# Kernel optimization log

Measured on AMD Instinct MI355X. Metric: run time of the kernel, lower is better.

Reference implementation:

```python
import jax, jax.numpy as jnp
import numpy as np

# dims: B graphs of n nodes each (equal-size batch, matching ptr)
B, NPG, DIN, DEMB, EPN = 16, 2048, 128, 64, 16
N = B * NPG
E = N * EPN
GAMMA = 5.0   # DGM ln gamma (temperature on normalized affinities)
STD = 0.01    # noise std


def _entmax15_core(z):
    # exact 1.5-entmax along last axis (Peters & Martins), sort-based threshold
    z = 0.5 * z
    z = z - jnp.max(z, axis=-1, keepdims=True)
    zs = jnp.sort(z, axis=-1)[..., ::-1]                  # descending
    k = z.shape[-1]
    rho = jnp.arange(1, k + 1, dtype=z.dtype)
    mean = jnp.cumsum(zs, axis=-1) / rho
    meansq = jnp.cumsum(zs * zs, axis=-1) / rho
    ss = rho * (meansq - jnp.square(mean))
    delta = (1.0 - ss) / rho
    tau = mean - jnp.sqrt(jnp.clip(delta, 0.0))
    support = jnp.sum((tau <= zs).astype(jnp.int32), axis=-1, keepdims=True)
    tau_star = jnp.take_along_axis(tau, support - 1, axis=-1)
    return jnp.square(jnp.clip(z - tau_star, 0.0))


@jax.custom_vjp
def entmax15(z):
    return _entmax15_core(z)

def _e_fwd(z):
    y = _entmax15_core(z)
    return y, y

def _e_bwd(y, dy):
    g = jnp.sqrt(y)
    dz = dy * g
    q = jnp.sum(dz, axis=-1, keepdims=True) / jnp.sum(g, axis=-1, keepdims=True)
    return (dz - q * g,)

entmax15.defvjp(_e_fwd, _e_bwd)


def setup_inputs() -> dict:
    key = jax.random.key(0)
    ks = jax.random.split(key, 6)
    x = jax.random.normal(ks[0], (N, DIN), dtype=jnp.float32)
    # intra-graph random edges: local ids + per-graph offset
    g = jax.random.randint(ks[1], (2, E), 0, NPG)
    off = jnp.repeat(jnp.arange(B, dtype=jnp.int64) * NPG, E // B)
    edge_index = (g.astype(jnp.int64) + off[None, :])
    batch = jnp.repeat(jnp.arange(B, dtype=jnp.int64), NPG)
    ptr = jnp.arange(B + 1, dtype=jnp.int64) * NPG
    W_self = jax.random.normal(ks[2], (DIN, DEMB), dtype=jnp.float32) / np.sqrt(DIN).astype(np.float32)
    W_nei = jax.random.normal(ks[3], (DIN, DEMB), dtype=jnp.float32) / np.sqrt(DIN).astype(np.float32)
    b = jnp.zeros((DEMB,), dtype=jnp.float32)
    noise = jax.random.normal(ks[4], (B, NPG, NPG), dtype=jnp.float32) * STD
    return {"x": x, "edge_index": edge_index, "batch": batch, "ptr": ptr,
            "W_self": W_self, "W_nei": W_nei, "b": b, "noise": noise}


def reference(x, edge_index, batch, ptr, W_self, W_nei, b, noise):
    Ntot = x.shape[0]
    Bn = ptr.shape[0] - 1
    n = Ntot // Bn
    src, dst = edge_index[0], edge_index[1]
    # embed_f: one mean-aggregation GCN layer
    h = x @ W_self
    msg = (x @ W_nei)[src]
    agg = jax.ops.segment_sum(msg, dst, num_segments=Ntot)
    deg = jax.ops.segment_sum(jnp.ones((src.shape[0],), x.dtype), dst, num_segments=Ntot)
    x_aux = jax.nn.relu(h + agg / jnp.clip(deg, 1.0)[:, None] + b)
    # per-graph pairwise euclidean distance (equal-size graphs -> [B,n,d])
    xb = x_aux.reshape(Bn, n, -1)
    sq = jnp.sum(xb * xb, axis=-1)
    d2 = sq[:, :, None] + sq[:, None, :] - 2.0 * jnp.einsum('bnd,bmd->bnm', xb, xb)
    D = jnp.sqrt(jnp.clip(d2, 0.0) + 1e-12)
    logits = -D + noise                              # noisy negative distances
    mu = jnp.mean(logits, axis=-1, keepdims=True)    # ln = LayerNorm(gamma)
    sd = jnp.std(logits, axis=-1, keepdims=True)
    A = entmax15(GAMMA * (logits - mu) / (sd + 1e-5))  # sparse edge probs [B,n,n]
    logprobs = jnp.log(A + 1e-6)
    return x_aux, A, logprobs
```

## Files before the change

### kernel.cpp

```cpp
#include <hip/hip_runtime.h>

#define NGRAPH 16
#define NPG    2048
#define NNODE  (NGRAPH*NPG)
#define DIN    128
#define DEMB   64
#define NEDGE  (NNODE*16)
#define QCAP   4096

__device__ __forceinline__ float wsum(float v) {
    #pragma unroll
    for (int m = 1; m < 64; m <<= 1) v += __shfl_xor(v, m, 64);
    return v;
}
__device__ __forceinline__ float wmax(float v) {
    #pragma unroll
    for (int m = 1; m < 64; m <<= 1) v = fmaxf(v, __shfl_xor(v, m, 64));
    return v;
}

__global__ __launch_bounds__(256) void k_inproj(
    const float* __restrict__ x, const float* __restrict__ Wself,
    const float* __restrict__ Wnei, float* __restrict__ h, float* __restrict__ xn)
{
    __shared__ float ws[DIN*DEMB];
    __shared__ float wn[DIN*DEMB];
    int tid = threadIdx.x;
    int n0 = blockIdx.x * 32;
    #pragma unroll
    for (int k = 0; k < 8; ++k) {
        ((float4*)ws)[tid + k*256] = ((const float4*)Wself)[tid + k*256];
        ((float4*)wn)[tid + k*256] = ((const float4*)Wnei)[tid + k*256];
    }
    __syncthreads();
    int nl = tid >> 3, og = (tid & 7) * 8;
    const float* xr = x + (size_t)(n0 + nl) * DIN;
    float ah[8] = {0,0,0,0,0,0,0,0};
    float an[8] = {0,0,0,0,0,0,0,0};
    for (int d4 = 0; d4 < DIN/4; ++d4) {
        float4 xv = *(const float4*)(xr + d4*4);
        #pragma unroll
        for (int dd = 0; dd < 4; ++dd) {
            float xs = (dd==0)?xv.x:(dd==1)?xv.y:(dd==2)?xv.z:xv.w;
            int d = d4*4 + dd;
            float4 a = *(const float4*)&ws[d*DEMB + og];
            float4 b = *(const float4*)&ws[d*DEMB + og + 4];
            ah[0] += xs*a.x; ah[1] += xs*a.y; ah[2] += xs*a.z; ah[3] += xs*a.w;
            ah[4] += xs*b.x; ah[5] += xs*b.y; ah[6] += xs*b.z; ah[7] += xs*b.w;
            float4 c = *(const float4*)&wn[d*DEMB + og];
            float4 e = *(const float4*)&wn[d*DEMB + og + 4];
            an[0] += xs*c.x; an[1] += xs*c.y; an[2] += xs*c.z; an[3] += xs*c.w;
            an[4] += xs*e.x; an[5] += xs*e.y; an[6] += xs*e.z; an[7] += xs*e.w;
        }
    }
    size_t o = (size_t)(n0 + nl)*DEMB + og;
    *(float4*)&h[o]    = make_float4(ah[0],ah[1],ah[2],ah[3]);
    *(float4*)&h[o+4]  = make_float4(ah[4],ah[5],ah[6],ah[7]);
    *(float4*)&xn[o]   = make_float4(an[0],an[1],an[2],an[3]);
    *(float4*)&xn[o+4] = make_float4(an[4],an[5],an[6],an[7]);
}

__global__ __launch_bounds__(1024) void k_agg(
    const int* __restrict__ ei, const float* __restrict__ xn,
    float* __restrict__ agg, float* __restrict__ deg)
{
    __shared__ float accL[128*64];
    __shared__ float degL[128];
    __shared__ int   queue[QCAP];
    __shared__ int   qcnt;
    int tid = threadIdx.x;
    int g   = blockIdx.x >> 4;
    int dlo = (blockIdx.x & 15) * 128;
    for (int k = tid; k < 128*64; k += 1024) accL[k] = 0.f;
    if (tid < 128) degL[tid] = 0.f;
    if (tid == 0) qcnt = 0;
    __syncthreads();
    int e0 = g * (NPG*16);
    int gbase = g * NPG;
    for (int k = 0; k < 32; ++k) {
        int e = e0 + k*1024 + tid;
        int dst = ei[NEDGE + e];
        int dl = dst - gbase - dlo;
        if ((unsigned)dl < 128u) {
            int src = ei[e];
            int qi = atomicAdd(&qcnt, 1);
            if (qi < QCAP) queue[qi] = (dl << 16) | src;
        }
    }
    __syncthreads();
    int qn = qcnt < QCAP ? qcnt : QCAP;
    int w = tid >> 6, l = tid & 63;
    int i = w;
    for (; i + 48 < qn; i += 64) {
        int p0 = queue[i], p1 = queue[i+16], p2 = queue[i+32], p3 = queue[i+48];
        float v0 = xn[(size_t)(p0 & 0xffff)*64 + l];
        float v1 = xn[(size_t)(p1 & 0xffff)*64 + l];
        float v2 = xn[(size_t)(p2 & 0xffff)*64 + l];
        float v3 = xn[(size_t)(p3 & 0xffff)*64 + l];
        atomicAdd(&accL[(p0 >> 16)*64 + l], v0);
        atomicAdd(&accL[(p1 >> 16)*64 + l], v1);
        atomicAdd(&accL[(p2 >> 16)*64 + l], v2);
        atomicAdd(&accL[(p3 >> 16)*64 + l], v3);
        if (l == 0) {
            atomicAdd(&degL[p0 >> 16], 1.f);
            atomicAdd(&degL[p1 >> 16], 1.f);
            atomicAdd(&degL[p2 >> 16], 1.f);
            atomicAdd(&degL[p3 >> 16], 1.f);
        }
    }
    for (; i < qn; i += 16) {
        int p0 = queue[i];
        float v0 = xn[(size_t)(p0 & 0xffff)*64 + l];
        atomicAdd(&accL[(p0 >> 16)*64 + l], v0);
        if (l == 0) atomicAdd(&degL[p0 >> 16], 1.f);
    }
    __syncthreads();
    size_t obase = (size_t)(gbase + dlo) * 64;
    for (int k = tid; k < 128*64; k += 1024) agg[obase + k] = accL[k];
    if (tid < 128) deg[gbase + dlo + tid] = degL[tid];
}

__global__ __launch_bounds__(256) void k_epi(
    const float* __restrict__ h, const float* __restrict__ agg,
    const float* __restrict__ deg, const float* __restrict__ bias,
    float* __restrict__ xaux, float* __restrict__ sqv)
{
    int w = threadIdx.x >> 6, l = threadIdx.x & 63;
    int n = blockIdx.x*4 + w;
    float dg = fmaxf(deg[n], 1.f);
    float v = h[(size_t)n*64 + l] + agg[(size_t)n*64 + l] / dg + bias[l];
    v = fmaxf(v, 0.f);
    xaux[(size_t)n*64 + l] = v;
    float s = wsum(v*v);
    if (l == 0) sqv[n] = s;
}

__global__ __launch_bounds__(256) void k_tr(
    const float* __restrict__ xaux, float* __restrict__ xtg)
{
    __shared__ float tl[64*65];
    int tid = threadIdx.x;
    int n0 = blockIdx.x * 64;
    #pragma unroll
    for (int k = 0; k < 16; ++k) {
        int e = tid + k*256;
        tl[(e >> 6)*65 + (e & 63)] = xaux[(size_t)n0*64 + e];
    }
    __syncthreads();
    #pragma unroll
    for (int k = 0; k < 16; ++k) {
        int f = tid + k*256;
        xtg[(size_t)(f >> 6)*NNODE + n0 + (f & 63)] = tl[(f & 63)*65 + (f >> 6)];
    }
}

#define PFMA(R, XI) { float xs_ = (XI); acc[R][0] += xs_*xj.x; acc[R][1] += xs_*xj.y; acc[R][2] += xs_*xj.z; acc[R][3] += xs_*xj.w; }

__global__ __launch_bounds__(512, 4) void k_pair(
    const float* __restrict__ xtg, const float* __restrict__ xaux,
    const float* __restrict__ sq, const float* __restrict__ noise,
    float* __restrict__ outA, float* __restrict__ outL)
{
    __shared__ float buf[4*2048];
    __shared__ float xit[64*8];
    __shared__ float sqi[8];
    int tid = threadIdx.x;
    int b  = blockIdx.x >> 8;
    int r0 = (blockIdx.x & 255) << 3;
    {
        int r = tid & 7, d = tid >> 3;
        xit[d*8 + r] = xaux[(size_t)(b*NPG + r0 + r)*64 + d];
        if (tid < 8) sqi[tid] = sq[b*NPG + r0 + tid];
    }
    __syncthreads();
    int w = tid >> 6, l = tid & 63;
    int jb = b*NPG + (w << 8) + (l << 2);

    float acc[8][4];
    #pragma unroll
    for (int r = 0; r < 8; ++r) { acc[r][0]=0.f; acc[r][1]=0.f; acc[r][2]=0.f; acc[r][3]=0.f; }

    const float* xp = xtg + jb;
    #pragma unroll 4
    for (int d = 0; d < 64; ++d) {
        float4 xj  = *(const float4*)(xp + (size_t)d*NNODE);
        float4 xiA = *(const float4*)&xit[d*8];
        float4 xiB = *(const float4*)&xit[d*8 + 4];
        PFMA(0, xiA.x) PFMA(1, xiA.y) PFMA(2, xiA.z) PFMA(3, xiA.w)
        PFMA(4, xiB.x) PFMA(5, xiB.y) PFMA(6, xiB.z) PFMA(7, xiB.w)
    }

    float4 sj = *(const float4*)&sq[jb];
    #pragma unroll
    for (int r = 0; r < 8; ++r) {
        float4 nz = *(const float4*)(noise + (size_t)(b*NPG + r0 + r)*NPG + (w << 8) + (l << 2));
        float si = sqi[r];
        acc[r][0] = nz.x - sqrtf(fmaxf(si + sj.x - 2.f*acc[r][0], 0.f) + 1e-12f);
        acc[r][1] = nz.y - sqrtf(fmaxf(si + sj.y - 2.f*acc[r][1], 0.f) + 1e-12f);
        acc[r][2] = nz.z - sqrtf(fmaxf(si + sj.z - 2.f*acc[r][2], 0.f) + 1e-12f);
        acc[r][3] = nz.w - sqrtf(fmaxf(si + sj.w - 2.f*acc[r][3], 0.f) + 1e-12f);
    }

    int col = (w << 8) + (l << 2);
    float z[8][4];
    int wr = w & 3;
    #pragma unroll
    for (int r = 0; r < 4; ++r)
        *(float4*)&buf[r*2048 + col] = make_float4(acc[r][0],acc[r][1],acc[r][2],acc[r][3]);
    __syncthreads();
    if (w < 4) {
        #pragma unroll
        for (int k = 0; k < 8; ++k) {
            float4 t = *(const float4*)&buf[wr*2048 + k*256 + (l << 2)];
            z[k][0]=t.x; z[k][1]=t.y; z[k][2]=t.z; z[k][3]=t.w;
        }
    }
    __syncthreads();
    #pragma unroll
    for (int r = 0; r < 4; ++r)
        *(float4*)&buf[r*2048 + col] = make_float4(acc[r+4][0],acc[r+4][1],acc[r+4][2],acc[r+4][3]);
    __syncthreads();
    if (w >= 4) {
        #pragma unroll
        for (int k = 0; k < 8; ++k) {
            float4 t = *(const float4*)&buf[wr*2048 + k*256 + (l << 2)];
            z[k][0]=t.x; z[k][1]=t.y; z[k][2]=t.z; z[k][3]=t.w;
        }
    }

    float s = 0.f;
    #pragma unroll
    for (int k = 0; k < 8; ++k) { s += z[k][0]; s += z[k][1]; s += z[k][2]; s += z[k][3]; }
    s = wsum(s);
    float mu = s * (1.f/2048.f);
    float vs = 0.f;
    #pragma unroll
    for (int k = 0; k < 8; ++k) {
        #pragma unroll
        for (int c = 0; c < 4; ++c) { float t = z[k][c] - mu; vs += t*t; }
    }
    vs = wsum(vs);
    float sd = sqrtf(vs * (1.f/2048.f));
    float mx = -1e30f;
    #pragma unroll
    for (int k = 0; k < 8; ++k) {
        #pragma unroll
        for (int c = 0; c < 4; ++c) mx = fmaxf(mx, z[k][c]);
    }
    mx = wmax(mx);

    float cc = 2.5f / (sd + 1e-5f);
    #pragma unroll
    for (int k = 0; k < 8; ++k) {
        #pragma unroll
        for (int c = 0; c < 4; ++c) z[k][c] = cc * (z[k][c] - mx);
    }

    float c0=-2.f, c1=-2.f, c2=-2.f, c3=-2.f; int cnt = 0;
    #pragma unroll
    for (int k = 0; k < 8; ++k) {
        #pragma unroll
        for (int c = 0; c < 4; ++c) {
            float zv = z[k][c];
            bool p = zv > -1.f;
            c3 = p ? c2 : c3; c2 = p ? c1 : c2; c1 = p ? c0 : c1; c0 = p ? zv : c0;
            cnt += p ? 1 : 0;
        }
    }
    unsigned long long ovf = __ballot(cnt > 4);

    float lo = -1.f, hi = 0.f;
    if (ovf == 0ull) {
        for (int it = 0; it < 25; ++it) {
            float mid = 0.5f*(lo+hi);
            float p, S;
            p = fmaxf(c0-mid,0.f); S  = p*p;
            p = fmaxf(c1-mid,0.f); S += p*p;
            p = fmaxf(c2-mid,0.f); S += p*p;
            p = fmaxf(c3-mid,0.f); S += p*p;
            S = wsum(S);
            bool ge = S >= 1.f;
            lo = ge ? mid : lo; hi = ge ? hi : mid;
        }
    } else {
        for (int it = 0; it < 25; ++it) {
            float mid = 0.5f*(lo+hi);
            float S = 0.f;
            #pragma unroll
            for (int k = 0; k < 8; ++k) {
                #pragma unroll
                for (int c = 0; c < 4; ++c) { float p = fmaxf(z[k][c]-mid, 0.f); S += p*p; }
            }
            S = wsum(S);
            bool ge = S >= 1.f;
            lo = ge ? mid : lo; hi = ge ? hi : mid;
        }
    }
    float tmid = 0.5f*(lo+hi);

    float k1 = 0.f, s1 = 0.f, q1 = 0.f;
    if (ovf == 0ull) {
        bool in;
        in = c0 > tmid; k1 += in?1.f:0.f; s1 += in?c0:0.f; q1 += in?c0*c0:0.f;
        in = c1 > tmid; k1 += in?1.f:0.f; s1 += in?c1:0.f; q1 += in?c1*c1:0.f;
        in = c2 > tmid; k1 += in?1.f:0.f; s1 += in?c2:0.f; q1 += in?c2*c2:0.f;
        in = c3 > tmid; k1 += in?1.f:0.f; s1 += in?c3:0.f; q1 += in?c3*c3:0.f;
    } else {
        #pragma unroll
        for (int k = 0; k < 8; ++k) {
            #pragma unroll
            for (int c = 0; c < 4; ++c) {
                float zv = z[k][c];
                bool in = zv > tmid;
                k1 += in?1.f:0.f; s1 += in?zv:0.f; q1 += in?zv*zv:0.f;
            }
        }
    }
    k1 = wsum(k1); s1 = wsum(s1); q1 = wsum(q1);
    float kin  = 1.f / k1;
    float mean = s1 * kin;
    float ssv  = q1 - s1*s1*kin;
    float tau  = mean - sqrtf(fmaxf((1.f - ssv)*kin, 0.f));

    size_t ro = (size_t)(b*NPG + r0 + w) * NPG;
    #pragma unroll
    for (int k = 0; k < 8; ++k) {
        float a0, a1, a2, a3, p;
        p = fmaxf(z[k][0]-tau, 0.f); a0 = p*p;
        p = fmaxf(z[k][1]-tau, 0.f); a1 = p*p;
        p = fmaxf(z[k][2]-tau, 0.f); a2 = p*p;
        p = fmaxf(z[k][3]-tau, 0.f); a3 = p*p;
        *(float4*)&outA[ro + k*256 + (l << 2)] = make_float4(a0,a1,a2,a3);
        *(float4*)&outL[ro + k*256 + (l << 2)] =
            make_float4(__logf(a0+1e-6f), __logf(a1+1e-6f), __logf(a2+1e-6f), __logf(a3+1e-6f));
    }
}

extern "C" void kernel_launch(void* const* d_in, const int* in_sizes, int n_in,
                              void* d_out, int out_size, void* d_ws, size_t ws_size,
                              hipStream_t stream)
{
    (void)in_sizes; (void)n_in; (void)out_size; (void)ws_size;
    const float* x     = (const float*)d_in[0];
    const int*   ei    = (const int*)d_in[1];
    const float* Wself = (const float*)d_in[4];
    const float* Wnei  = (const float*)d_in[5];
    const float* bias  = (const float*)d_in[6];
    const float* noise = (const float*)d_in[7];
    float* out = (float*)d_out;
    float* ws  = (float*)d_ws;

    float* h    = ws;
    float* xn   = ws + 2097152;
    float* agg  = ws + 4194304;
    float* deg  = ws + 6291456;
    float* sqv  = ws + 6324224;
    float* xtg  = h;

    float* xaux = out;
    float* outA = out + 2097152;
    float* outL = out + 69206016;

    hipLaunchKernelGGL(k_inproj, dim3(1024), dim3(256), 0, stream, x, Wself, Wnei, h, xn);
    hipLaunchKernelGGL(k_agg,    dim3(256),  dim3(1024), 0, stream, ei, xn, agg, deg);
    hipLaunchKernelGGL(k_epi,    dim3(8192), dim3(256), 0, stream, h, agg, deg, bias, xaux, sqv);
    hipLaunchKernelGGL(k_tr,     dim3(512),  dim3(256), 0, stream, xaux, xtg);
    hipLaunchKernelGGL(k_pair,   dim3(4096), dim3(512), 0, stream, xtg, xaux, sqv, noise, outA, outL);
}
```

Baseline: 1.101 ms.

## Double pair-kernel row tile, fuse epilogue with transpose, add nontemporal I/O

The pairwise kernel now handles 16 rows per block instead of 8, so each loaded xj column is reused across twice as many rows and the grid is halved. Entmax runs twice per block through a new helper. The epilogue and transpose kernels are merged into one, which drops a launch and the xaux re-read. Noise loads and the A/logprob stores use nontemporal hints, the agg gather loop is unrolled 8-wide, and xtg gets its own workspace slot because h is now read in the same kernel that writes xtg. The larger accumulator array raises register pressure and may lower occupancy under the 512x4 launch bound.

```diff
diff --git a/kernel.cpp b/kernel.cpp
--- a/kernel.cpp
+++ b/kernel.cpp
@@ -7,6 +7,8 @@
 #define DEMB   64
 #define NEDGE  (NNODE*16)
 #define QCAP   4096
+
+typedef float f32x4 __attribute__((ext_vector_type(4)));
 
 __device__ __forceinline__ float wsum(float v) {
     #pragma unroll
@@ -91,21 +93,16 @@
     int qn = qcnt < QCAP ? qcnt : QCAP;
     int w = tid >> 6, l = tid & 63;
     int i = w;
-    for (; i + 48 < qn; i += 64) {
-        int p0 = queue[i], p1 = queue[i+16], p2 = queue[i+32], p3 = queue[i+48];
-        float v0 = xn[(size_t)(p0 & 0xffff)*64 + l];
-        float v1 = xn[(size_t)(p1 & 0xffff)*64 + l];
-        float v2 = xn[(size_t)(p2 & 0xffff)*64 + l];
-        float v3 = xn[(size_t)(p3 & 0xffff)*64 + l];
-        atomicAdd(&accL[(p0 >> 16)*64 + l], v0);
-        atomicAdd(&accL[(p1 >> 16)*64 + l], v1);
-        atomicAdd(&accL[(p2 >> 16)*64 + l], v2);
-        atomicAdd(&accL[(p3 >> 16)*64 + l], v3);
-        if (l == 0) {
-            atomicAdd(&degL[p0 >> 16], 1.f);
-            atomicAdd(&degL[p1 >> 16], 1.f);
-            atomicAdd(&degL[p2 >> 16], 1.f);
-            atomicAdd(&degL[p3 >> 16], 1.f);
+    for (; i + 112 < qn; i += 128) {
+        int p[8]; float v[8];
+        #pragma unroll
+        for (int k = 0; k < 8; ++k) p[k] = queue[i + 16*k];
+        #pragma unroll
+        for (int k = 0; k < 8; ++k) v[k] = xn[(size_t)(p[k] & 0xffff)*64 + l];
+        #pragma unroll
+        for (int k = 0; k < 8; ++k) {
+            atomicAdd(&accL[(p[k] >> 16)*64 + l], v[k]);
+            if (l == 0) atomicAdd(&degL[p[k] >> 16], 1.f);
         }
     }
     for (; i < qn; i += 16) {
@@ -120,31 +117,26 @@
     if (tid < 128) deg[gbase + dlo + tid] = degL[tid];
 }
 
-__global__ __launch_bounds__(256) void k_epi(
+__global__ __launch_bounds__(256) void k_epitr(
     const float* __restrict__ h, const float* __restrict__ agg,
     const float* __restrict__ deg, const float* __restrict__ bias,
-    float* __restrict__ xaux, float* __restrict__ sqv)
-{
-    int w = threadIdx.x >> 6, l = threadIdx.x & 63;
-    int n = blockIdx.x*4 + w;
-    float dg = fmaxf(deg[n], 1.f);
-    float v = h[(size_t)n*64 + l] + agg[(size_t)n*64 + l] / dg + bias[l];
-    v = fmaxf(v, 0.f);
-    xaux[(size_t)n*64 + l] = v;
-    float s = wsum(v*v);
-    if (l == 0) sqv[n] = s;
-}
-
-__global__ __launch_bounds__(256) void k_tr(
-    const float* __restrict__ xaux, float* __restrict__ xtg)
+    float* __restrict__ xaux, float* __restrict__ sqv, float* __restrict__ xtg)
 {
     __shared__ float tl[64*65];
     int tid = threadIdx.x;
     int n0 = blockIdx.x * 64;
+    int w = tid >> 6, l = tid & 63;
     #pragma unroll
     for (int k = 0; k < 16; ++k) {
-        int e = tid + k*256;
-        tl[(e >> 6)*65 + (e & 63)] = xaux[(size_t)n0*64 + e];
+        int n = k*4 + w;
+        float dg = fmaxf(deg[n0 + n], 1.f);
+        size_t ge = (size_t)(n0 + n)*64 + l;
+        float v = h[ge] + agg[ge] / dg + bias[l];
+        v = fmaxf(v, 0.f);
+        xaux[ge] = v;
+        float s = wsum(v*v);
+        if (l == 0) sqv[n0 + n] = s;
+        tl[n*65 + l] = v;
     }
     __syncthreads();
     #pragma unroll
@@ -156,78 +148,9 @@
 
 #define PFMA(R, XI) { float xs_ = (XI); acc[R][0] += xs_*xj.x; acc[R][1] += xs_*xj.y; acc[R][2] += xs_*xj.z; acc[R][3] += xs_*xj.w; }
 
-__global__ __launch_bounds__(512, 4) void k_pair(
-    const float* __restrict__ xtg, const float* __restrict__ xaux,
-    const float* __restrict__ sq, const float* __restrict__ noise,
-    float* __restrict__ outA, float* __restrict__ outL)
-{
-    __shared__ float buf[4*2048];
-    __shared__ float xit[64*8];
-    __shared__ float sqi[8];
-    int tid = threadIdx.x;
-    int b  = blockIdx.x >> 8;
-    int r0 = (blockIdx.x & 255) << 3;
-    {
-        int r = tid & 7, d = tid >> 3;
-        xit[d*8 + r] = xaux[(size_t)(b*NPG + r0 + r)*64 + d];
-        if (tid < 8) sqi[tid] = sq[b*NPG + r0 + tid];
-    }
-    __syncthreads();
-    int w = tid >> 6, l = tid & 63;
-    int jb = b*NPG + (w << 8) + (l << 2);
-
-    float acc[8][4];
-    #pragma unroll
-    for (int r = 0; r < 8; ++r) { acc[r][0]=0.f; acc[r][1]=0.f; acc[r][2]=0.f; acc[r][3]=0.f; }
-
-    const float* xp = xtg + jb;
-    #pragma unroll 4
-    for (int d = 0; d < 64; ++d) {
-        float4 xj  = *(const float4*)(xp + (size_t)d*NNODE);
-        float4 xiA = *(const float4*)&xit[d*8];
-        float4 xiB = *(const float4*)&xit[d*8 + 4];
-        PFMA(0, xiA.x) PFMA(1, xiA.y) PFMA(2, xiA.z) PFMA(3, xiA.w)
-        PFMA(4, xiB.x) PFMA(5, xiB.y) PFMA(6, xiB.z) PFMA(7, xiB.w)
-    }
-
-    float4 sj = *(const float4*)&sq[jb];
-    #pragma unroll
-    for (int r = 0; r < 8; ++r) {
-        float4 nz = *(const float4*)(noise + (size_t)(b*NPG + r0 + r)*NPG + (w << 8) + (l << 2));
-        float si = sqi[r];
-        acc[r][0] = nz.x - sqrtf(fmaxf(si + sj.x - 2.f*acc[r][0], 0.f) + 1e-12f);
-        acc[r][1] = nz.y - sqrtf(fmaxf(si + sj.y - 2.f*acc[r][1], 0.f) + 1e-12f);
-        acc[r][2] = nz.z - sqrtf(fmaxf(si + sj.z - 2.f*acc[r][2], 0.f) + 1e-12f);
-        acc[r][3] = nz.w - sqrtf(fmaxf(si + sj.w - 2.f*acc[r][3], 0.f) + 1e-12f);
-    }
-
-    int col = (w << 8) + (l << 2);
-    float z[8][4];
-    int wr = w & 3;
-    #pragma unroll
-    for (int r = 0; r < 4; ++r)
-        *(float4*)&buf[r*2048 + col] = make_float4(acc[r][0],acc[r][1],acc[r][2],acc[r][3]);
-    __syncthreads();
-    if (w < 4) {
-        #pragma unroll
-        for (int k = 0; k < 8; ++k) {
-            float4 t = *(const float4*)&buf[wr*2048 + k*256 + (l << 2)];
-            z[k][0]=t.x; z[k][1]=t.y; z[k][2]=t.z; z[k][3]=t.w;
-        }
-    }
-    __syncthreads();
-    #pragma unroll
-    for (int r = 0; r < 4; ++r)
-        *(float4*)&buf[r*2048 + col] = make_float4(acc[r+4][0],acc[r+4][1],acc[r+4][2],acc[r+4][3]);
-    __syncthreads();
-    if (w >= 4) {
-        #pragma unroll
-        for (int k = 0; k < 8; ++k) {
-            float4 t = *(const float4*)&buf[wr*2048 + k*256 + (l << 2)];
-            z[k][0]=t.x; z[k][1]=t.y; z[k][2]=t.z; z[k][3]=t.w;
-        }
-    }
-
+__device__ __forceinline__ void entmax_row(
+    float (&z)[8][4], int l, size_t ro, float* __restrict__ outA, float* __restrict__ outL)
+{
     float s = 0.f;
     #pragma unroll
     for (int k = 0; k < 8; ++k) { s += z[k][0]; s += z[k][1]; s += z[k][2]; s += z[k][3]; }
@@ -322,18 +245,125 @@
     float ssv  = q1 - s1*s1*kin;
     float tau  = mean - sqrtf(fmaxf((1.f - ssv)*kin, 0.f));
 
-    size_t ro = (size_t)(b*NPG + r0 + w) * NPG;
-    #pragma unroll
-    for (int k = 0; k < 8; ++k) {
-        float a0, a1, a2, a3, p;
-        p = fmaxf(z[k][0]-tau, 0.f); a0 = p*p;
-        p = fmaxf(z[k][1]-tau, 0.f); a1 = p*p;
-        p = fmaxf(z[k][2]-tau, 0.f); a2 = p*p;
-        p = fmaxf(z[k][3]-tau, 0.f); a3 = p*p;
-        *(float4*)&outA[ro + k*256 + (l << 2)] = make_float4(a0,a1,a2,a3);
-        *(float4*)&outL[ro + k*256 + (l << 2)] =
-            make_float4(__logf(a0+1e-6f), __logf(a1+1e-6f), __logf(a2+1e-6f), __logf(a3+1e-6f));
-    }
+    #pragma unroll
+    for (int k = 0; k < 8; ++k) {
+        float p;
+        f32x4 a, lg;
+        p = fmaxf(z[k][0]-tau, 0.f); a.x = p*p;
+        p = fmaxf(z[k][1]-tau, 0.f); a.y = p*p;
+        p = fmaxf(z[k][2]-tau, 0.f); a.z = p*p;
+        p = fmaxf(z[k][3]-tau, 0.f); a.w = p*p;
+        lg.x = __logf(a.x+1e-6f); lg.y = __logf(a.y+1e-6f);
+        lg.z = __logf(a.z+1e-6f); lg.w = __logf(a.w+1e-6f);
+        __builtin_nontemporal_store(a,  (f32x4*)&outA[ro + k*256 + (l << 2)]);
+        __builtin_nontemporal_store(lg, (f32x4*)&outL[ro + k*256 + (l << 2)]);
+    }
+}
+
+__global__ __launch_bounds__(512, 4) void k_pair(
+    const float* __restrict__ xtg, const float* __restrict__ xaux,
+    const float* __restrict__ sq, const float* __restrict__ noise,
+    float* __restrict__ outA, float* __restrict__ outL)
+{
+    __shared__ float buf[4*2048];
+    __shared__ float xit[64*16];
+    __shared__ float sqi[16];
+    int tid = threadIdx.x;
+    int b  = blockIdx.x >> 7;
+    int r0 = (blockIdx.x & 127) << 4;
+    {
+        int e = tid;
+        xit[e] = xaux[(size_t)(b*NPG + r0 + (e & 15))*64 + (e >> 4)];
+        e = tid + 512;
+        xit[e] = xaux[(size_t)(b*NPG + r0 + (e & 15))*64 + (e >> 4)];
+        if (tid < 16) sqi[tid] = sq[b*NPG + r0 + tid];
+    }
+    __syncthreads();
+    int w = tid >> 6, l = tid & 63;
+    int jb = b*NPG + (w << 8) + (l << 2);
+
+    float acc[16][4];
+    #pragma unroll
+    for (int r = 0; r < 16; ++r) { acc[r][0]=0.f; acc[r][1]=0.f; acc[r][2]=0.f; acc[r][3]=0.f; }
+
+    const float* xp = xtg + jb;
+    #pragma unroll 2
+    for (int d = 0; d < 64; ++d) {
+        float4 xj = *(const float4*)(xp + (size_t)d*NNODE);
+        const float4* xi = (const float4*)&xit[d*16];
+        float4 x0 = xi[0], x1 = xi[1], x2 = xi[2], x3 = xi[3];
+        PFMA( 0,x0.x) PFMA( 1,x0.y) PFMA( 2,x0.z) PFMA( 3,x0.w)
+        PFMA( 4,x1.x) PFMA( 5,x1.y) PFMA( 6,x1.z) PFMA( 7,x1.w)
+        PFMA( 8,x2.x) PFMA( 9,x2.y) PFMA(10,x2.z) PFMA(11,x2.w)
+        PFMA(12,x3.x) PFMA(13,x3.y) PFMA(14,x3.z) PFMA(15,x3.w)
+    }
+
+    float4 sj = *(const float4*)&sq[jb];
+    #pragma unroll
+    for (int r = 0; r < 16; ++r) {
+        f32x4 nz = __builtin_nontemporal_load(
+            (const f32x4*)(noise + (size_t)(b*NPG + r0 + r)*NPG + (w << 8) + (l << 2)));
+        float si = sqi[r];
+        acc[r][0] = nz.x - sqrtf(fmaxf(si + sj.x - 2.f*acc[r][0], 0.f) + 1e-12f);
+        acc[r][1] = nz.y - sqrtf(fmaxf(si + sj.y - 2.f*acc[r][1], 0.f) + 1e-12f);
+        acc[r][2] = nz.z - sqrtf(fmaxf(si + sj.z - 2.f*acc[r][2], 0.f) + 1e-12f);
+        acc[r][3] = nz.w - sqrtf(fmaxf(si + sj.w - 2.f*acc[r][3], 0.f) + 1e-12f);
+    }
+
+    int col = (w << 8) + (l << 2);
+    int wr = w & 3;
+    float z[8][4];
+
+    #pragma unroll
+    for (int r = 0; r < 4; ++r)
+        *(float4*)&buf[r*2048 + col] = make_float4(acc[r][0],acc[r][1],acc[r][2],acc[r][3]);
+    __syncthreads();
+    if (w < 4) {
+        #pragma unroll
+        for (int k = 0; k < 8; ++k) {
+            float4 t = *(const float4*)&buf[wr*2048 + k*256 + (l << 2)];
+            z[k][0]=t.x; z[k][1]=t.y; z[k][2]=t.z; z[k][3]=t.w;
+        }
+    }
+    __syncthreads();
+    #pragma unroll
+    for (int r = 0; r < 4; ++r)
+        *(float4*)&buf[r*2048 + col] = make_float4(acc[r+4][0],acc[r+4][1],acc[r+4][2],acc[r+4][3]);
+    __syncthreads();
+    if (w >= 4) {
+        #pragma unroll
+        for (int k = 0; k < 8; ++k) {
+            float4 t = *(const float4*)&buf[wr*2048 + k*256 + (l << 2)];
+            z[k][0]=t.x; z[k][1]=t.y; z[k][2]=t.z; z[k][3]=t.w;
+        }
+    }
+    __syncthreads();
+    entmax_row(z, l, (size_t)(b*NPG + r0 + w) * NPG, outA, outL);
+
+    #pragma unroll
+    for (int r = 0; r < 4; ++r)
+        *(float4*)&buf[r*2048 + col] = make_float4(acc[r+8][0],acc[r+8][1],acc[r+8][2],acc[r+8][3]);
+    __syncthreads();
+    if (w < 4) {
+        #pragma unroll
+        for (int k = 0; k < 8; ++k) {
+            float4 t = *(const float4*)&buf[wr*2048 + k*256 + (l << 2)];
+            z[k][0]=t.x; z[k][1]=t.y; z[k][2]=t.z; z[k][3]=t.w;
+        }
+    }
+    __syncthreads();
+    #pragma unroll
+    for (int r = 0; r < 4; ++r)
+        *(float4*)&buf[r*2048 + col] = make_float4(acc[r+12][0],acc[r+12][1],acc[r+12][2],acc[r+12][3]);
+    __syncthreads();
+    if (w >= 4) {
+        #pragma unroll
+        for (int k = 0; k < 8; ++k) {
+            float4 t = *(const float4*)&buf[wr*2048 + k*256 + (l << 2)];
+            z[k][0]=t.x; z[k][1]=t.y; z[k][2]=t.z; z[k][3]=t.w;
+        }
+    }
+    entmax_row(z, l, (size_t)(b*NPG + r0 + 8 + w) * NPG, outA, outL);
 }
 
 extern "C" void kernel_launch(void* const* d_in, const int* in_sizes, int n_in,
@@ -355,15 +385,14 @@
     float* agg  = ws + 4194304;
     float* deg  = ws + 6291456;
     float* sqv  = ws + 6324224;
-    float* xtg  = h;
+    float* xtg  = ws + 6356992;
 
     float* xaux = out;
     float* outA = out + 2097152;
     float* outL = out + 69206016;
 
-    hipLaunchKernelGGL(k_inproj, dim3(1024), dim3(256), 0, stream, x, Wself, Wnei, h, xn);
+    hipLaunchKernelGGL(k_inproj, dim3(1024), dim3(256),  0, stream, x, Wself, Wnei, h, xn);
     hipLaunchKernelGGL(k_agg,    dim3(256),  dim3(1024), 0, stream, ei, xn, agg, deg);
-    hipLaunchKernelGGL(k_epi,    dim3(8192), dim3(256), 0, stream, h, agg, deg, bias, xaux, sqv);
-    hipLaunchKernelGGL(k_tr,     dim3(512),  dim3(256), 0, stream, xaux, xtg);
-    hipLaunchKernelGGL(k_pair,   dim3(4096), dim3(512), 0, stream, xtg, xaux, sqv, noise, outA, outL);
-}
+    hipLaunchKernelGGL(k_epitr,  dim3(512),  dim3(256),  0, stream, h, agg, deg, bias, xaux, sqv, xtg);
+    hipLaunchKernelGGL(k_pair,   dim3(2048), dim3(512),  0, stream, xtg, xaux, sqv, noise, outA, outL);
+}
```

Measured after the change: 1.185 ms. 1.08x slower.
